# Kernel tuning notes

Hardware: AMD Instinct MI355X
Metric: run time of the kernel (lower is better)

The kernel has to match this reference:

```python
import jax, jax.numpy as jnp
import numpy as np

B, N, F_IN, H, OUT = 64, 1024, 195, 128, 64
K1, K2 = N // 2, N // 4  # ceil(0.5*N), ceil(0.5*K1)
EPS = 1e-5


def setup_inputs() -> dict:
    key = jax.random.key(0)
    ks = jax.random.split(key, 16)
    rn = lambda k, s: jax.random.normal(k, s, dtype=jnp.float32) * 0.1
    inp = {
        "input": jax.random.normal(ks[0], (B, N, F_IN), dtype=jnp.float32),
        # SAGEConv1 (195->128): lin_l (neighbors, w/ bias), lin_r (root, no bias)
        "W1l": rn(ks[1], (H, F_IN)), "b1l": jnp.zeros((H,), jnp.float32),
        "W1r": rn(ks[2], (H, F_IN)),
        # SAGPooling1 GNN = GraphConv(128->1): lin_rel (sum aggr, w/ bias), lin_root (no bias)
        "Wp1_rel": rn(ks[3], (1, H)), "bp1_rel": jnp.zeros((1,), jnp.float32),
        "Wp1_root": rn(ks[4], (1, H)),
        # SAGEConv2 (128->64)
        "W2l": rn(ks[5], (OUT, H)), "b2l": jnp.zeros((OUT,), jnp.float32),
        "W2r": rn(ks[6], (OUT, H)),
        # SAGPooling2 GNN = GraphConv(64->1)
        "Wp2_rel": rn(ks[7], (1, OUT)), "bp2_rel": jnp.zeros((1,), jnp.float32),
        "Wp2_root": rn(ks[8], (1, OUT)),
        # MLP head
        "fc1_w": rn(ks[9], (512, OUT)), "fc1_b": jnp.zeros((512,), jnp.float32),
        "bn1_g": jnp.ones((512,), jnp.float32), "bn1_b": jnp.zeros((512,), jnp.float32),
        "bn1_m": jnp.zeros((512,), jnp.float32), "bn1_v": jnp.ones((512,), jnp.float32),
        "fc2_w": rn(ks[10], (256, 512)), "fc2_b": jnp.zeros((256,), jnp.float32),
        "bn2_g": jnp.ones((256,), jnp.float32), "bn2_b": jnp.zeros((256,), jnp.float32),
        "bn2_m": jnp.zeros((256,), jnp.float32), "bn2_v": jnp.ones((256,), jnp.float32),
        "fc3_w": rn(ks[11], (2, 256)), "fc3_b": jnp.zeros((2,), jnp.float32),
    }
    return inp


def _corr_adj(x):
    # Pearson corrcoef over rows of x [B,N,F] -> boolean adjacency [B,N,N] (corr > 0.5)
    xc = x - x.mean(axis=-1, keepdims=True)
    cov = jnp.einsum("bnf,bmf->bnm", xc, xc)
    d = jnp.sqrt(jnp.clip(jnp.einsum("bnnf->bn", cov[..., None] * 0 + 0) + jnp.diagonal(cov, axis1=1, axis2=2), 1e-12))
    corr = cov / (d[:, :, None] * d[:, None, :])
    return (corr > 0.5).astype(x.dtype)  # symmetric, includes self-loops


def _sage(x, A, Wl, bl, Wr):
    # PyG SAGEConv: lin_l(mean_{j in N(i)} x_j) + lin_r(x_i)
    deg = A.sum(axis=-1, keepdims=True)
    agg = jnp.einsum("bnm,bmf->bnf", A, x) / jnp.maximum(deg, 1.0)
    return jnp.einsum("bnf,hf->bnh", agg, Wl) + bl + jnp.einsum("bnf,hf->bnh", x, Wr)


def _sagpool(x, A, Wrel, brel, Wroot, k):
    # score via GraphConv (sum aggr): lin_rel(sum_j x_j) + lin_root(x_i)
    agg = jnp.einsum("bnm,bmf->bnf", A, x)
    score = (jnp.einsum("bnf,of->bno", agg, Wrel) + brel
             + jnp.einsum("bnf,of->bno", x, Wroot))[..., 0]  # [B,N]
    top_s, idx = jax.lax.top_k(score, k)  # per-graph top-k nodes
    x_new = jnp.take_along_axis(x, idx[:, :, None], axis=1) * jnp.tanh(top_s)[:, :, None]
    A_new = jnp.take_along_axis(A, idx[:, :, None], axis=1)
    A_new = jnp.take_along_axis(A_new, idx[:, None, :], axis=2)
    return x_new, A_new


def _bn_eval(x, g, b, m, v):
    return g * (x - m) * jax.lax.rsqrt(v + EPS) + b


def reference(input, W1l, b1l, W1r, Wp1_rel, bp1_rel, Wp1_root,
              W2l, b2l, W2r, Wp2_rel, bp2_rel, Wp2_root,
              fc1_w, fc1_b, bn1_g, bn1_b, bn1_m, bn1_v,
              fc2_w, fc2_b, bn2_g, bn2_b, bn2_m, bn2_v,
              fc3_w, fc3_b):
    A = _corr_adj(input)                                   # [B,N,N]
    x = jax.nn.relu(_sage(input, A, W1l, b1l, W1r))        # [B,N,128]
    x, A = _sagpool(x, A, Wp1_rel, bp1_rel, Wp1_root, K1)  # [B,K1,128]
    x = jax.nn.relu(_sage(x, A, W2l, b2l, W2r))            # [B,K1,64]
    x, A = _sagpool(x, A, Wp2_rel, bp2_rel, Wp2_root, K2)  # [B,K2,64]
    x = x.mean(axis=1)                                     # global mean pool -> [B,64]
    x = _bn_eval(jax.nn.relu(x @ fc1_w.T + fc1_b), bn1_g, bn1_b, bn1_m, bn1_v)
    x = _bn_eval(jax.nn.relu(x @ fc2_w.T + fc2_b), bn2_g, bn2_b, bn2_m, bn2_v)
    x = x @ fc3_w.T + fc3_b
    return jax.nn.softmax(x, axis=1)
```

## Files before the change

kernel.cpp:

```cpp
#include <hip/hip_runtime.h>
#include <cstdint>


typedef __bf16 bf16x8 __attribute__((ext_vector_type(8)));
typedef float  floatx4 __attribute__((ext_vector_type(4)));

#define MFMA_BF16(a, b, c) __builtin_amdgcn_mfma_f32_16x16x32_bf16((a), (b), (c), 0, 0, 0)

static constexpr int BATCH = 64, NNODE = 1024, FIN = 195, FPAD = 224;
static constexpr int HD = 128, OD = 64, KP1 = 512, KP2 = 256;

static constexpr size_t OFF_GHI   = 0;
static constexpr size_t OFF_GLO   = 8388608;
static constexpr size_t OFF_A1B   = 16777216;
static constexpr size_t OFF_YR2   = 18874368;
static constexpr size_t OFF_X2    = 35651584;
static constexpr size_t OFF_XHI   = 0;
static constexpr size_t OFF_XLO   = 29360128;
static constexpr size_t OFF_ABITS = 58720256;
static constexpr size_t OFF_X1    = 67108864;
static constexpr size_t OFF_P1    = 100663296;
static constexpr size_t OFF_Q1    = OFF_P1 + 262144;
static constexpr size_t OFF_IDX1  = OFF_Q1 + 262144;
static constexpr size_t OFF_GATE1 = OFF_IDX1 + 131072;
static constexpr size_t OFF_P2    = OFF_GATE1 + 131072;
static constexpr size_t OFF_Q2    = OFF_P2 + 131072;
static constexpr size_t OFF_W1HI  = OFF_Q2 + 131072;
static constexpr size_t OFF_W1LO  = OFF_W1HI + 114688;
static constexpr size_t OFF_W2HI  = OFF_W1LO + 114688;
static constexpr size_t OFF_W2LO  = OFF_W2HI + 32768;
static constexpr size_t OFF_XHAT  = 102760448;
static constexpr size_t OFF_YR1   = 102760448;

__global__ __launch_bounds__(256) void prep_pack_kernel(
    const float* __restrict__ x, __bf16* __restrict__ xhi,
    __bf16* __restrict__ xlo, __bf16* __restrict__ xhat,
    const float* __restrict__ W1l, const float* __restrict__ W1r,
    __bf16* __restrict__ hi1, __bf16* __restrict__ lo1,
    const float* __restrict__ W2l, const float* __restrict__ W2r,
    __bf16* __restrict__ hi2, __bf16* __restrict__ lo2) {
  int bid = blockIdx.x;
  if (bid < 16384) {
    int row  = bid * 4 + (threadIdx.x >> 6);
    int lane = threadIdx.x & 63;
    const float* xr = x + (long)row * FIN;
    int k0 = lane * 4;
    float v[4];
#pragma unroll
    for (int i = 0; i < 4; ++i) v[i] = (k0 + i < FIN) ? xr[k0 + i] : 0.f;
    float s = v[0] + v[1] + v[2] + v[3];
#pragma unroll
    for (int o = 32; o; o >>= 1) s += __shfl_xor(s, o);
    float mean = s * (1.f / (float)FIN);
    float c[4], ss = 0.f;
#pragma unroll
    for (int i = 0; i < 4; ++i) {
      c[i] = (k0 + i < FIN) ? (v[i] - mean) : 0.f;
      ss += c[i] * c[i];
    }
#pragma unroll
    for (int o = 32; o; o >>= 1) ss += __shfl_xor(ss, o);
    float inv = rsqrtf(fmaxf(ss, 1e-12f));
    if (k0 < FPAD) {
      __bf16 hi4[4], lo4[4], hat4[4];
#pragma unroll
      for (int i = 0; i < 4; ++i) {
        float xv = (k0 + i < FIN) ? v[i] : 0.f;
        __bf16 h = (__bf16)xv;
        hi4[i] = h;
        lo4[i] = (__bf16)(xv - (float)h);
        hat4[i] = (__bf16)(c[i] * inv);
      }
      long base = (long)row * FPAD + k0;
      *(uint2*)&xhi[base]  = *(const uint2*)hi4;
      *(uint2*)&xlo[base]  = *(const uint2*)lo4;
      *(uint2*)&xhat[base] = *(const uint2*)hat4;
    }
  } else if (bid < 16384 + 224) {
    int idx = (bid - 16384) * 256 + threadIdx.x;
    int h = idx / FPAD, k = idx % FPAD;
    float v = 0.f;
    if (k < FIN) v = (h < HD) ? W1l[h * FIN + k] : W1r[(h - HD) * FIN + k];
    __bf16 a = (__bf16)v;
    hi1[idx] = a;
    lo1[idx] = (__bf16)(v - (float)a);
  } else {
    int idx = (bid - 16384 - 224) * 256 + threadIdx.x;
    int h = idx / HD, k = idx % HD;
    float v = (h < OD) ? W2l[h * HD + k] : W2r[(h - OD) * HD + k];
    __bf16 a = (__bf16)v;
    hi2[idx] = a;
    lo2[idx] = (__bf16)(v - (float)a);
  }
}

static constexpr int CK = 40;
__global__ __launch_bounds__(256) void corr_kernel(
    const __bf16* __restrict__ xhat, unsigned short* __restrict__ Abits) {
  __shared__ __align__(16) __bf16 sI[128 * CK];
  __shared__ __align__(16) __bf16 sJ[128 * CK];
  int bid = blockIdx.x;
  int xcd = bid & 7;
  int m = bid >> 3;
  int b = xcd + ((m & 7) << 3);
  int rem = m >> 3, bi = 0;
  while (rem >= 8 - bi) { rem -= 8 - bi; ++bi; }
  int bj = bi + rem;
  int i0 = bi * 128, j0 = bj * 128;
  const __bf16* Xb = xhat + (long)b * NNODE * FPAD;
  int lane = threadIdx.x & 63, wave = threadIdx.x >> 6;
  int wi = (wave >> 1) * 64, wj = (wave & 1) * 64;
  int lr = lane & 15, lk = (lane >> 4) * 8;
  int strow = threadIdx.x & 127;
  int stc = (threadIdx.x >> 7) * 8;
  floatx4 zero = {0.f, 0.f, 0.f, 0.f};
  floatx4 acc[4][4];
#pragma unroll
  for (int i = 0; i < 4; ++i)
#pragma unroll
    for (int j = 0; j < 4; ++j) acc[i][j] = zero;
  for (int kk = 0; kk < 7; ++kk) {
    int k0 = kk * 32;
    __syncthreads();
    {
      const __bf16* gI = Xb + (long)(i0 + strow) * FPAD + k0;
      const __bf16* gJ = Xb + (long)(j0 + strow) * FPAD + k0;
      *(uint4*)&sI[strow * CK + stc]      = *(const uint4*)(gI + stc);
      *(uint4*)&sI[strow * CK + stc + 16] = *(const uint4*)(gI + stc + 16);
      *(uint4*)&sJ[strow * CK + stc]      = *(const uint4*)(gJ + stc);
      *(uint4*)&sJ[strow * CK + stc + 16] = *(const uint4*)(gJ + stc + 16);
    }
    __syncthreads();
    bf16x8 af[4], bf[4];
#pragma unroll
    for (int t = 0; t < 4; ++t) {
      af[t] = *(const bf16x8*)&sI[(wi + t * 16 + lr) * CK + lk];
      bf[t] = *(const bf16x8*)&sJ[(wj + t * 16 + lr) * CK + lk];
    }
#pragma unroll
    for (int ti = 0; ti < 4; ++ti)
#pragma unroll
      for (int tj = 0; tj < 4; ++tj)
        acc[ti][tj] = MFMA_BF16(af[ti], bf[tj], acc[ti][tj]);
  }
#pragma unroll
  for (int ti = 0; ti < 4; ++ti)
#pragma unroll
    for (int tj = 0; tj < 4; ++tj) {
      floatx4 a = acc[ti][tj];
      unsigned long long m0 = __ballot(a[0] > 0.5f);
      unsigned long long m1 = __ballot(a[1] > 0.5f);
      unsigned long long m2 = __ballot(a[2] > 0.5f);
      unsigned long long m3 = __ballot(a[3] > 0.5f);
      if (lane < 16) {
        unsigned long long mm = (lane & 2) ? ((lane & 1) ? m3 : m2)
                                           : ((lane & 1) ? m1 : m0);
        unsigned short piece = (unsigned short)(mm >> ((lane >> 2) * 16));
        int grow = i0 + wi + ti * 16 + lane;
        int gcol = (j0 + wj + tj * 16) >> 4;
        Abits[((long)b * NNODE + grow) * 64 + gcol] = piece;
      }
    }
}

template <int K, int NCOL>
__global__ __launch_bounds__(512, 2) void gemm_split_kernel(
    const __bf16* __restrict__ Ahi, const __bf16* __restrict__ Alo,
    const __bf16* __restrict__ Bhi, const __bf16* __restrict__ Blo,
    float* __restrict__ C, int mblocks,
    unsigned long long* __restrict__ A64, int ntrans) {
  constexpr int ldc = NCOL * 128;
  int bid = blockIdx.x;
  if (bid >= mblocks * NCOL) {
    int t = bid - mblocks * NCOL;
    if (t >= ntrans || threadIdx.x >= 256) return;
    int b = t / 28, pi = t % 28;
    int rem = pi, rb = 1;
    while (rem >= rb) { rem -= rb; ++rb; }
    int cb = rem;
    int wave = threadIdx.x >> 6, lane = threadIdx.x & 63;
    int dr = rb * 2 + (wave >> 1);
    int dc = cb * 2 + (wave & 1);
    long base = (long)b * NNODE;
    unsigned long long xv = A64[(base + dc * 64 + lane) * 16 + dr];
    const unsigned long long M1  = 0x5555555555555555ULL;
    const unsigned long long M2  = 0x3333333333333333ULL;
    const unsigned long long M4  = 0x0F0F0F0F0F0F0F0FULL;
    const unsigned long long M8  = 0x00FF00FF00FF00FFULL;
    const unsigned long long M16 = 0x0000FFFF0000FFFFULL;
    const unsigned long long M32 = 0x00000000FFFFFFFFULL;
#define TSTEP(Kk, M)                                                      \
    {                                                                     \
      unsigned long long y = __shfl_xor(xv, Kk);                          \
      xv = ((lane & Kk) == 0) ? ((xv & (M)) | ((y & (M)) << Kk))          \
                              : ((xv & ~(M)) | ((y & ~(M)) >> Kk));       \
    }
    TSTEP(1, M1) TSTEP(2, M2) TSTEP(4, M4) TSTEP(8, M8) TSTEP(16, M16) TSTEP(32, M32)
#undef TSTEP
    A64[(base + dr * 64 + lane) * 16 + dc] = xv;
    return;
  }
  int mrow, col;
  if (NCOL == 2) {
    int xcd = bid & 7;
    int q = bid >> 3;
    col = q & 1;
    mrow = (xcd << 6) + (q >> 1);
  } else {
    mrow = bid;
    col = 0;
  }
  long row0 = (long)mrow * 128;
  int col0 = col * 128;
  int lane = threadIdx.x & 63, wave = threadIdx.x >> 6;
  int wi = (wave >> 1) * 32, wj = (wave & 1) * 64;
  int lr = lane & 15, lk = (lane >> 4) * 8;
  const __bf16* pAh = Ahi + (row0 + wi + lr) * (long)K + lk;
  const __bf16* pAl = Alo + (row0 + wi + lr) * (long)K + lk;
  const __bf16* pBh = Bhi + (long)(col0 + wj + lr) * K + lk;
  const __bf16* pBl = Blo + (long)(col0 + wj + lr) * K + lk;
  floatx4 zero = {0.f, 0.f, 0.f, 0.f};
  floatx4 acc[2][4];
#pragma unroll
  for (int i = 0; i < 2; ++i)
#pragma unroll
    for (int j = 0; j < 4; ++j) acc[i][j] = zero;
#pragma unroll
  for (int kk = 0; kk < (K >> 5); ++kk) {
    int k0 = kk * 32;
    bf16x8 ah[2], al[2], bh[4], bl[4];
#pragma unroll
    for (int t = 0; t < 2; ++t) {
      ah[t] = *(const bf16x8*)(pAh + (long)t * 16 * K + k0);
      al[t] = *(const bf16x8*)(pAl + (long)t * 16 * K + k0);
    }
#pragma unroll
    for (int t = 0; t < 4; ++t) {
      bh[t] = *(const bf16x8*)(pBh + (long)t * 16 * K + k0);
      bl[t] = *(const bf16x8*)(pBl + (long)t * 16 * K + k0);
    }
#pragma unroll
    for (int tj = 0; tj < 4; ++tj)
#pragma unroll
      for (int ti = 0; ti < 2; ++ti) {
        acc[ti][tj] = MFMA_BF16(ah[ti], bh[tj], acc[ti][tj]);
        acc[ti][tj] = MFMA_BF16(ah[ti], bl[tj], acc[ti][tj]);
        acc[ti][tj] = MFMA_BF16(al[ti], bh[tj], acc[ti][tj]);
      }
  }
#pragma unroll
  for (int ti = 0; ti < 2; ++ti)
#pragma unroll
    for (int tj = 0; tj < 4; ++tj)
#pragma unroll
      for (int rr = 0; rr < 4; ++rr) {
        long grow = row0 + wi + ti * 16 + (lane >> 4) * 4 + rr;
        int gcol = col0 + wj + tj * 16 + (lane & 15);
        C[grow * ldc + gcol] = acc[ti][tj][rr];
      }
}

__global__ __launch_bounds__(256) void sage1_kernel(
    const unsigned int* __restrict__ Abits32, const float* __restrict__ YR1,
    const float* __restrict__ b1l, const float* __restrict__ Wrel,
    const float* __restrict__ Wroot, float* __restrict__ x1,
    float* __restrict__ p1, float* __restrict__ q1) {
  int half = threadIdx.x >> 7;
  int node = blockIdx.x * 2 + half;
  int b = node >> 10;
  int h = threadIdx.x & 127;
  __shared__ int list[2][1024];
  __shared__ int s_deg[2];
  __shared__ float redp[2][2], redq[2][2];
  if (h < 32) {
    unsigned int word = Abits32[(long)node * 32 + h];
    int cnt = __popc(word);
    int off = cnt;
#pragma unroll
    for (int o = 1; o < 32; o <<= 1) {
      int v = __shfl_up(off, o);
      if (h >= o) off += v;
    }
    off -= cnt;
    if (h == 31) s_deg[half] = off + cnt;
    int basei = h * 32;
    while (word) {
      int t = __ffs(word) - 1;
      word &= word - 1;
      list[half][off++] = basei + t;
    }
  }
  __syncthreads();
  int deg = s_deg[half];
  long ybase = (long)(b << 10) * 256;
  float accv = 0.f;
  for (int d = 0; d < deg; ++d)
    accv += YR1[ybase + (long)list[half][d] * 256 + h];
  float R = YR1[(long)node * 256 + 128 + h];
  float v = accv / (float)(deg < 1 ? 1 : deg) + b1l[h] + R;
  v = fmaxf(v, 0.f);
  x1[(long)node * 128 + h] = v;
  float pv = v * Wrel[h], qv = v * Wroot[h];
#pragma unroll
  for (int o = 32; o; o >>= 1) { pv += __shfl_xor(pv, o); qv += __shfl_xor(qv, o); }
  int wv = h >> 6, lane = h & 63;
  if (lane == 0) { redp[half][wv] = pv; redq[half][wv] = qv; }
  __syncthreads();
  if (h == 0) {
    p1[node] = redp[half][0] + redp[half][1];
    q1[node] = redq[half][0] + redq[half][1];
  }
}

__global__ void scoretopk_kernel(const unsigned int* __restrict__ bits32,
                                 const float* __restrict__ p,
                                 const float* __restrict__ q,
                                 const float* __restrict__ brel,
                                 int* __restrict__ idx_out,
                                 float* __restrict__ gate_out,
                                 int nwords, int rpb_shift, int k) {
  int b = blockIdx.x, tid = threadIdx.x;
  int row = (b << rpb_shift) + tid;
  const unsigned int* wptr = bits32 + (long)row * nwords;
  const float* pb = p + ((long)b << rpb_shift);
  float s = q[row] + brel[0];
  for (int w = 0; w < nwords; ++w) {
    unsigned int word = wptr[w];
    while (word) {
      int t = __ffs(word) - 1;
      word &= word - 1;
      s += pb[w * 32 + t];
    }
  }
  unsigned int fb = __float_as_uint(s);
  unsigned int key = (fb & 0x80000000u) ? ~fb : (fb | 0x80000000u);
  __shared__ int hist[256];
  __shared__ unsigned int sh_prefix;
  __shared__ int sh_target, cnt_gt, cnt_eq, outpos;
  if (tid == 0) { sh_prefix = 0; sh_target = k; cnt_gt = 0; cnt_eq = 0; outpos = 0; }
  for (int shift = 24; shift >= 0; shift -= 8) {
    if (tid < 256) hist[tid] = 0;
    __syncthreads();
    unsigned int prefix = sh_prefix;
    bool inset = (shift == 24) || ((key >> (shift + 8)) == (prefix >> (shift + 8)));
    if (inset) atomicAdd(&hist[(key >> shift) & 255], 1);
    __syncthreads();
    if (tid < 64) {
      int lane = tid;
      int bb0 = hist[255 - 4 * lane];
      int bb1 = hist[254 - 4 * lane];
      int bb2 = hist[253 - 4 * lane];
      int bb3 = hist[252 - 4 * lane];
      int c0 = bb0, c1 = c0 + bb1, c2 = c1 + bb2, c3 = c2 + bb3;
      int incl = c3;
#pragma unroll
      for (int o = 1; o < 64; o <<= 1) {
        int v = __shfl_up(incl, o);
        if (lane >= o) incl += v;
      }
      int excl = incl - c3;
      int target = sh_target;
      int cum[4] = {excl + c0, excl + c1, excl + c2, excl + c3};
      int prev = excl;
#pragma unroll
      for (int i = 0; i < 4; ++i) {
        if (cum[i] >= target && prev < target) {
          int bin = 255 - (4 * lane + i);
          sh_prefix = prefix | ((unsigned int)bin << shift);
          sh_target = target - prev;
        }
        prev = cum[i];
      }
    }
    __syncthreads();
  }
  unsigned int T = sh_prefix;
  if (key > T) atomicAdd(&cnt_gt, 1);
  __syncthreads();
  int E = k - cnt_gt;
  bool sel = (key > T);
  if (!sel && key == T) sel = (atomicAdd(&cnt_eq, 1) < E);
  if (sel) {
    int posn = atomicAdd(&outpos, 1);
    idx_out[b * k + posn] = tid;
    gate_out[b * k + posn] = tanhf(s);
  }
}

__global__ __launch_bounds__(256) void gather_kernel(
    const float* __restrict__ x1, const int* __restrict__ idx,
    const float* __restrict__ gate, __bf16* __restrict__ ghi,
    __bf16* __restrict__ glo, const unsigned int* __restrict__ Abits32,
    unsigned long long* __restrict__ A1bits) {
  int bid = blockIdx.x;
  if (bid < 16384) {
    long e = (long)bid * 256 + threadIdx.x;
    int h = (int)(e & 127);
    int i = (int)((e >> 7) & 511);
    int b = (int)(e >> 16);
    int srow = idx[(b << 9) + i];
    float v = x1[((long)(b << 10) + srow) * 128 + h] * gate[(b << 9) + i];
    __bf16 a = (__bf16)v;
    ghi[e] = a;
    glo[e] = (__bf16)(v - (float)a);
  } else {
    int gi = (bid - 16384) * 4 + (threadIdx.x >> 6);
    int lane = threadIdx.x & 63;
    int b = gi >> 9;
    int srow = idx[gi];
    const unsigned int* src = Abits32 + ((long)(b << 10) + srow) * 32;
    const int* idxb = idx + (b << 9);
#pragma unroll
    for (int t = 0; t < 8; ++t) {
      int cj = idxb[t * 64 + lane];
      int bit = (src[cj >> 5] >> (cj & 31)) & 1;
      unsigned long long m = __ballot(bit);
      if (lane == 0) A1bits[(long)gi * 8 + t] = m;
    }
  }
}

__global__ __launch_bounds__(256) void sage2_kernel(
    const unsigned int* __restrict__ A1b32, const float* __restrict__ YR2,
    const float* __restrict__ b2l, const float* __restrict__ Wrel,
    const float* __restrict__ Wroot, float* __restrict__ x2,
    float* __restrict__ p2, float* __restrict__ q2) {
  int qw = threadIdx.x >> 6;
  int row = blockIdx.x * 4 + qw;
  int b = row >> 9;
  int h = threadIdx.x & 63;
  __shared__ int list[4][512];
  __shared__ int s_deg[4];
  if (h < 16) {
    unsigned int word = A1b32[(long)row * 16 + h];
    int cnt = __popc(word);
    int off = cnt;
#pragma unroll
    for (int o = 1; o < 16; o <<= 1) {
      int v = __shfl_up(off, o);
      if (h >= o) off += v;
    }
    off -= cnt;
    if (h == 15) s_deg[qw] = off + cnt;
    int basei = h * 32;
    while (word) {
      int t = __ffs(word) - 1;
      word &= word - 1;
      list[qw][off++] = basei + t;
    }
  }
  __syncthreads();
  int deg = s_deg[qw];
  long ybase = (long)(b << 9) * 128;
  float accv = 0.f;
  for (int d = 0; d < deg; ++d)
    accv += YR2[ybase + (long)list[qw][d] * 128 + h];
  float R = YR2[(long)row * 128 + 64 + h];
  float v = fmaxf(accv / (float)(deg < 1 ? 1 : deg) + b2l[h] + R, 0.f);
  x2[(long)row * 64 + h] = v;
  float pv = v * Wrel[h], qv = v * Wroot[h];
#pragma unroll
  for (int o = 32; o; o >>= 1) { pv += __shfl_xor(pv, o); qv += __shfl_xor(qv, o); }
  if (h == 0) { p2[row] = pv; q2[row] = qv; }
}

__global__ __launch_bounds__(512) void scoretopk_head_kernel(
    const unsigned int* __restrict__ A1b32, const float* __restrict__ p2,
    const float* __restrict__ q2, const float* __restrict__ brel,
    const float* __restrict__ x2, const float* __restrict__ fc1_w,
    const float* __restrict__ fc1_b, const float* __restrict__ g1,
    const float* __restrict__ bb1, const float* __restrict__ m1,
    const float* __restrict__ v1, const float* __restrict__ fc2_w,
    const float* __restrict__ fc2_b, const float* __restrict__ g2,
    const float* __restrict__ bb2, const float* __restrict__ m2,
    const float* __restrict__ v2, const float* __restrict__ fc3_w,
    const float* __restrict__ fc3_b, float* __restrict__ out) {
  int b = blockIdx.x, tid = threadIdx.x;
  int row = (b << 9) + tid;
  const unsigned int* wptr = A1b32 + (long)row * 16;
  const float* pb = p2 + ((long)b << 9);
  float s = q2[row] + brel[0];
  for (int w = 0; w < 16; ++w) {
    unsigned int word = wptr[w];
    while (word) {
      int t = __ffs(word) - 1;
      word &= word - 1;
      s += pb[w * 32 + t];
    }
  }
  constexpr int k = KP2;
  unsigned int fb = __float_as_uint(s);
  unsigned int key = (fb & 0x80000000u) ? ~fb : (fb | 0x80000000u);
  __shared__ int hist[256];
  __shared__ int idx2s[256];
  __shared__ float gate2s[256];
  __shared__ unsigned int sh_prefix;
  __shared__ int sh_target, cnt_gt, cnt_eq, outpos;
  if (tid == 0) { sh_prefix = 0; sh_target = k; cnt_gt = 0; cnt_eq = 0; outpos = 0; }
  for (int shift = 24; shift >= 0; shift -= 8) {
    if (tid < 256) hist[tid] = 0;
    __syncthreads();
    unsigned int prefix = sh_prefix;
    bool inset = (shift == 24) || ((key >> (shift + 8)) == (prefix >> (shift + 8)));
    if (inset) atomicAdd(&hist[(key >> shift) & 255], 1);
    __syncthreads();
    if (tid < 64) {
      int lane = tid;
      int bb0 = hist[255 - 4 * lane];
      int bb1 = hist[254 - 4 * lane];
      int bb2 = hist[253 - 4 * lane];
      int bb3 = hist[252 - 4 * lane];
      int c0 = bb0, c1 = c0 + bb1, c2 = c1 + bb2, c3 = c2 + bb3;
      int incl = c3;
#pragma unroll
      for (int o = 1; o < 64; o <<= 1) {
        int v = __shfl_up(incl, o);
        if (lane >= o) incl += v;
      }
      int excl = incl - c3;
      int target = sh_target;
      int cum[4] = {excl + c0, excl + c1, excl + c2, excl + c3};
      int prev = excl;
#pragma unroll
      for (int i = 0; i < 4; ++i) {
        if (cum[i] >= target && prev < target) {
          int bin = 255 - (4 * lane + i);
          sh_prefix = prefix | ((unsigned int)bin << shift);
          sh_target = target - prev;
        }
        prev = cum[i];
      }
    }
    __syncthreads();
  }
  unsigned int T = sh_prefix;
  if (key > T) atomicAdd(&cnt_gt, 1);
  __syncthreads();
  int E = k - cnt_gt;
  bool sel = (key > T);
  if (!sel && key == T) sel = (atomicAdd(&cnt_eq, 1) < E);
  if (sel) {
    int posn = atomicAdd(&outpos, 1);
    idx2s[posn] = tid;
    gate2s[posn] = tanhf(s);
  }
  __syncthreads();
  __shared__ float part[8][64];
  __shared__ float pooled[64];
  __shared__ float h1[512];
  __shared__ float h2[256];
  __shared__ float zz[2];
  int h = tid & 63, grp = tid >> 6;
  float sp = 0.f;
  for (int i = grp * 32; i < grp * 32 + 32; ++i) {
    int si = idx2s[i];
    sp += x2[((long)(b << 9) + si) * 64 + h] * gate2s[i];
  }
  part[grp][h] = sp;
  __syncthreads();
  if (tid < 64) {
    float t = 0.f;
#pragma unroll
    for (int g = 0; g < 8; ++g) t += part[g][tid];
    pooled[tid] = t * (1.f / 256.f);
  }
  __syncthreads();
  {
    float z = fc1_b[tid];
    for (int j = 0; j < 64; ++j) z += pooled[j] * fc1_w[tid * 64 + j];
    z = fmaxf(z, 0.f);
    h1[tid] = g1[tid] * (z - m1[tid]) * rsqrtf(v1[tid] + 1e-5f) + bb1[tid];
  }
  __syncthreads();
  if (tid < 256) {
    float z = fc2_b[tid];
    for (int j = 0; j < 512; ++j) z += h1[j] * fc2_w[tid * 512 + j];
    z = fmaxf(z, 0.f);
    h2[tid] = g2[tid] * (z - m2[tid]) * rsqrtf(v2[tid] + 1e-5f) + bb2[tid];
  }
  __syncthreads();
  if (tid < 2) {
    float z = fc3_b[tid];
    for (int j = 0; j < 256; ++j) z += h2[j] * fc3_w[tid * 256 + j];
    zz[tid] = z;
  }
  __syncthreads();
  if (tid == 0) {
    float mx = fmaxf(zz[0], zz[1]);
    float e0 = expf(zz[0] - mx), e1 = expf(zz[1] - mx);
    float inv = 1.f / (e0 + e1);
    out[b * 2 + 0] = e0 * inv;
    out[b * 2 + 1] = e1 * inv;
  }
}

extern "C" void kernel_launch(void* const* d_in, const int* in_sizes, int n_in,
                              void* d_out, int out_size, void* d_ws, size_t ws_size,
                              hipStream_t stream) {
  (void)in_sizes; (void)n_in; (void)out_size; (void)ws_size;
  const float* input   = (const float*)d_in[0];
  const float* W1l     = (const float*)d_in[1];
  const float* b1l     = (const float*)d_in[2];
  const float* W1r     = (const float*)d_in[3];
  const float* Wp1_rel = (const float*)d_in[4];
  const float* bp1_rel = (const float*)d_in[5];
  const float* Wp1_root= (const float*)d_in[6];
  const float* W2l     = (const float*)d_in[7];
  const float* b2l     = (const float*)d_in[8];
  const float* W2r     = (const float*)d_in[9];
  const float* Wp2_rel = (const float*)d_in[10];
  const float* bp2_rel = (const float*)d_in[11];
  const float* Wp2_root= (const float*)d_in[12];
  const float* fc1_w   = (const float*)d_in[13];
  const float* fc1_b   = (const float*)d_in[14];
  const float* bn1_g   = (const float*)d_in[15];
  const float* bn1_b   = (const float*)d_in[16];
  const float* bn1_m   = (const float*)d_in[17];
  const float* bn1_v   = (const float*)d_in[18];
  const float* fc2_w   = (const float*)d_in[19];
  const float* fc2_b   = (const float*)d_in[20];
  const float* bn2_g   = (const float*)d_in[21];
  const float* bn2_b   = (const float*)d_in[22];
  const float* bn2_m   = (const float*)d_in[23];
  const float* bn2_v   = (const float*)d_in[24];
  const float* fc3_w   = (const float*)d_in[25];
  const float* fc3_b   = (const float*)d_in[26];

  char* ws = (char*)d_ws;
  __bf16* xhi   = (__bf16*)(ws + OFF_XHI);
  __bf16* xlo   = (__bf16*)(ws + OFF_XLO);
  __bf16* xhat  = (__bf16*)(ws + OFF_XHAT);
  unsigned short* Abits = (unsigned short*)(ws + OFF_ABITS);
  const unsigned int* Abits32 = (const unsigned int*)(ws + OFF_ABITS);
  unsigned long long* A64 = (unsigned long long*)(ws + OFF_ABITS);
  float* YR1    = (float*)(ws + OFF_YR1);
  float* x1     = (float*)(ws + OFF_X1);
  float* p1     = (float*)(ws + OFF_P1);
  float* q1     = (float*)(ws + OFF_Q1);
  int*   idx1   = (int*)(ws + OFF_IDX1);
  float* gate1  = (float*)(ws + OFF_GATE1);
  float* p2     = (float*)(ws + OFF_P2);
  float* q2     = (float*)(ws + OFF_Q2);
  __bf16* w1hi  = (__bf16*)(ws + OFF_W1HI);
  __bf16* w1lo  = (__bf16*)(ws + OFF_W1LO);
  __bf16* w2hi  = (__bf16*)(ws + OFF_W2HI);
  __bf16* w2lo  = (__bf16*)(ws + OFF_W2LO);
  __bf16* ghi   = (__bf16*)(ws + OFF_GHI);
  __bf16* glo   = (__bf16*)(ws + OFF_GLO);
  unsigned long long* A1bits = (unsigned long long*)(ws + OFF_A1B);
  const unsigned int* A1b32  = (const unsigned int*)(ws + OFF_A1B);
  float* YR2    = (float*)(ws + OFF_YR2);
  float* x2     = (float*)(ws + OFF_X2);
  float* out    = (float*)d_out;

  prep_pack_kernel<<<16672, 256, 0, stream>>>(input, xhi, xlo, xhat,
                                              W1l, W1r, w1hi, w1lo,
                                              W2l, W2r, w2hi, w2lo);
  corr_kernel<<<2304, 256, 0, stream>>>(xhat, Abits);
  gemm_split_kernel<224, 2><<<1024 + 1792, 512, 0, stream>>>(
      xhi, xlo, w1hi, w1lo, YR1, 512, A64, 1792);
  sage1_kernel<<<32768, 256, 0, stream>>>(Abits32, YR1, b1l, Wp1_rel, Wp1_root, x1, p1, q1);
  scoretopk_kernel<<<64, 1024, 0, stream>>>(Abits32, p1, q1, bp1_rel, idx1, gate1,
                                            32, 10, KP1);
  gather_kernel<<<24576, 256, 0, stream>>>(x1, idx1, gate1, ghi, glo, Abits32, A1bits);
  gemm_split_kernel<128, 1><<<256, 512, 0, stream>>>(
      ghi, glo, w2hi, w2lo, YR2, 256, nullptr, 0);
  sage2_kernel<<<8192, 256, 0, stream>>>(A1b32, YR2, b2l, Wp2_rel, Wp2_root, x2, p2, q2);
  scoretopk_head_kernel<<<64, 512, 0, stream>>>(A1b32, p2, q2, bp2_rel, x2,
                                                fc1_w, fc1_b, bn1_g, bn1_b, bn1_m, bn1_v,
                                                fc2_w, fc2_b, bn2_g, bn2_b, bn2_m, bn2_v,
                                                fc3_w, fc3_b, out);
}
```

Baseline: 389.9 us.

## Compute correlation adjacency with FP8 MFMA and enlarge split-GEMM wave tiles

Normalized rows for the correlation matrix are now stored as FP8 e4m3 instead of bf16, and corr_kernel uses the fp8 16x16x32 MFMA. This halves the staging bytes and LDS traffic for the adjacency build. The threshold at 0.5 may flip for correlations near the boundary, because FP8 keeps only a 3-bit mantissa, so the result can diverge from the reference. Separately, gemm_split runs with 256 threads per block, each wave computing a 64x64 tile instead of 32x64, which raises register use and data reuse per wave. The YR1 offset is moved so it no longer aliases the xhat buffer.

```diff
diff --git a/kernel.cpp b/kernel.cpp
--- a/kernel.cpp
+++ b/kernel.cpp
@@ -1,4 +1,5 @@
 #include <hip/hip_runtime.h>
+#include <hip/hip_fp8.h>
 #include <cstdint>
 
 
@@ -6,6 +7,7 @@
 typedef float  floatx4 __attribute__((ext_vector_type(4)));
 
 #define MFMA_BF16(a, b, c) __builtin_amdgcn_mfma_f32_16x16x32_bf16((a), (b), (c), 0, 0, 0)
+#define MFMA_FP8(a, b, c)  __builtin_amdgcn_mfma_f32_16x16x32_fp8_fp8((a), (b), (c), 0, 0, 0)
 
 static constexpr int BATCH = 64, NNODE = 1024, FIN = 195, FPAD = 224;
 static constexpr int HD = 128, OD = 64, KP1 = 512, KP2 = 256;
@@ -30,11 +32,16 @@
 static constexpr size_t OFF_W2HI  = OFF_W1LO + 114688;
 static constexpr size_t OFF_W2LO  = OFF_W2HI + 32768;
 static constexpr size_t OFF_XHAT  = 102760448;
-static constexpr size_t OFF_YR1   = 102760448;
+static constexpr size_t OFF_YR1   = 102760448 + 16777216;
+
+static __device__ __forceinline__ unsigned char to_fp8(float v) {
+  __hip_fp8_e4m3 q(v);
+  return *(unsigned char*)&q;
+}
 
 __global__ __launch_bounds__(256) void prep_pack_kernel(
     const float* __restrict__ x, __bf16* __restrict__ xhi,
-    __bf16* __restrict__ xlo, __bf16* __restrict__ xhat,
+    __bf16* __restrict__ xlo, unsigned char* __restrict__ xhat8,
     const float* __restrict__ W1l, const float* __restrict__ W1r,
     __bf16* __restrict__ hi1, __bf16* __restrict__ lo1,
     const float* __restrict__ W2l, const float* __restrict__ W2r,
@@ -62,19 +69,20 @@
     for (int o = 32; o; o >>= 1) ss += __shfl_xor(ss, o);
     float inv = rsqrtf(fmaxf(ss, 1e-12f));
     if (k0 < FPAD) {
-      __bf16 hi4[4], lo4[4], hat4[4];
+      __bf16 hi4[4], lo4[4];
+      unsigned char h8[4];
 #pragma unroll
       for (int i = 0; i < 4; ++i) {
         float xv = (k0 + i < FIN) ? v[i] : 0.f;
         __bf16 h = (__bf16)xv;
         hi4[i] = h;
         lo4[i] = (__bf16)(xv - (float)h);
-        hat4[i] = (__bf16)(c[i] * inv);
+        h8[i] = to_fp8(c[i] * inv);
       }
       long base = (long)row * FPAD + k0;
-      *(uint2*)&xhi[base]  = *(const uint2*)hi4;
-      *(uint2*)&xlo[base]  = *(const uint2*)lo4;
-      *(uint2*)&xhat[base] = *(const uint2*)hat4;
+      *(uint2*)&xhi[base] = *(const uint2*)hi4;
+      *(uint2*)&xlo[base] = *(const uint2*)lo4;
+      *(unsigned int*)&xhat8[base] = *(const unsigned int*)h8;
     }
   } else if (bid < 16384 + 224) {
     int idx = (bid - 16384) * 256 + threadIdx.x;
@@ -94,11 +102,11 @@
   }
 }
 
-static constexpr int CK = 40;
+static constexpr int CKB = 48;
 __global__ __launch_bounds__(256) void corr_kernel(
-    const __bf16* __restrict__ xhat, unsigned short* __restrict__ Abits) {
-  __shared__ __align__(16) __bf16 sI[128 * CK];
-  __shared__ __align__(16) __bf16 sJ[128 * CK];
+    const unsigned char* __restrict__ xhat8, unsigned short* __restrict__ Abits) {
+  __shared__ __align__(16) unsigned char sI[128 * CKB];
+  __shared__ __align__(16) unsigned char sJ[128 * CKB];
   int bid = blockIdx.x;
   int xcd = bid & 7;
   int m = bid >> 3;
@@ -107,12 +115,12 @@
   while (rem >= 8 - bi) { rem -= 8 - bi; ++bi; }
   int bj = bi + rem;
   int i0 = bi * 128, j0 = bj * 128;
-  const __bf16* Xb = xhat + (long)b * NNODE * FPAD;
+  const unsigned char* Xb = xhat8 + (long)b * NNODE * FPAD;
   int lane = threadIdx.x & 63, wave = threadIdx.x >> 6;
   int wi = (wave >> 1) * 64, wj = (wave & 1) * 64;
-  int lr = lane & 15, lk = (lane >> 4) * 8;
+  int lr = lane & 15, lk8 = (lane >> 4) * 8;
   int strow = threadIdx.x & 127;
-  int stc = (threadIdx.x >> 7) * 8;
+  int sbuf = threadIdx.x >> 7;
   floatx4 zero = {0.f, 0.f, 0.f, 0.f};
   floatx4 acc[4][4];
 #pragma unroll
@@ -123,25 +131,23 @@
     int k0 = kk * 32;
     __syncthreads();
     {
-      const __bf16* gI = Xb + (long)(i0 + strow) * FPAD + k0;
-      const __bf16* gJ = Xb + (long)(j0 + strow) * FPAD + k0;
-      *(uint4*)&sI[strow * CK + stc]      = *(const uint4*)(gI + stc);
-      *(uint4*)&sI[strow * CK + stc + 16] = *(const uint4*)(gI + stc + 16);
-      *(uint4*)&sJ[strow * CK + stc]      = *(const uint4*)(gJ + stc);
-      *(uint4*)&sJ[strow * CK + stc + 16] = *(const uint4*)(gJ + stc + 16);
-    }
-    __syncthreads();
-    bf16x8 af[4], bf[4];
+      unsigned char* dst = (sbuf ? sJ : sI) + strow * CKB;
+      const unsigned char* src = Xb + (long)((sbuf ? j0 : i0) + strow) * FPAD + k0;
+      *(uint4*)(dst)      = *(const uint4*)(src);
+      *(uint4*)(dst + 16) = *(const uint4*)(src + 16);
+    }
+    __syncthreads();
+    long long af[4], bf[4];
 #pragma unroll
     for (int t = 0; t < 4; ++t) {
-      af[t] = *(const bf16x8*)&sI[(wi + t * 16 + lr) * CK + lk];
-      bf[t] = *(const bf16x8*)&sJ[(wj + t * 16 + lr) * CK + lk];
+      af[t] = *(const long long*)&sI[(wi + t * 16 + lr) * CKB + lk8];
+      bf[t] = *(const long long*)&sJ[(wj + t * 16 + lr) * CKB + lk8];
     }
 #pragma unroll
     for (int ti = 0; ti < 4; ++ti)
 #pragma unroll
       for (int tj = 0; tj < 4; ++tj)
-        acc[ti][tj] = MFMA_BF16(af[ti], bf[tj], acc[ti][tj]);
+        acc[ti][tj] = MFMA_FP8(af[ti], bf[tj], acc[ti][tj]);
   }
 #pragma unroll
   for (int ti = 0; ti < 4; ++ti)
@@ -164,7 +170,7 @@
 }
 
 template <int K, int NCOL>
-__global__ __launch_bounds__(512, 2) void gemm_split_kernel(
+__global__ __launch_bounds__(256, 2) void gemm_split_kernel(
     const __bf16* __restrict__ Ahi, const __bf16* __restrict__ Alo,
     const __bf16* __restrict__ Bhi, const __bf16* __restrict__ Blo,
     float* __restrict__ C, int mblocks,
@@ -173,7 +179,7 @@
   int bid = blockIdx.x;
   if (bid >= mblocks * NCOL) {
     int t = bid - mblocks * NCOL;
-    if (t >= ntrans || threadIdx.x >= 256) return;
+    if (t >= ntrans) return;
     int b = t / 28, pi = t % 28;
     int rem = pi, rb = 1;
     while (rem >= rb) { rem -= rb; ++rb; }
@@ -213,43 +219,40 @@
   long row0 = (long)mrow * 128;
   int col0 = col * 128;
   int lane = threadIdx.x & 63, wave = threadIdx.x >> 6;
-  int wi = (wave >> 1) * 32, wj = (wave & 1) * 64;
+  int wi = (wave >> 1) * 64, wj = (wave & 1) * 64;
   int lr = lane & 15, lk = (lane >> 4) * 8;
   const __bf16* pAh = Ahi + (row0 + wi + lr) * (long)K + lk;
   const __bf16* pAl = Alo + (row0 + wi + lr) * (long)K + lk;
   const __bf16* pBh = Bhi + (long)(col0 + wj + lr) * K + lk;
   const __bf16* pBl = Blo + (long)(col0 + wj + lr) * K + lk;
   floatx4 zero = {0.f, 0.f, 0.f, 0.f};
-  floatx4 acc[2][4];
-#pragma unroll
-  for (int i = 0; i < 2; ++i)
+  floatx4 acc[4][4];
+#pragma unroll
+  for (int i = 0; i < 4; ++i)
 #pragma unroll
     for (int j = 0; j < 4; ++j) acc[i][j] = zero;
 #pragma unroll
   for (int kk = 0; kk < (K >> 5); ++kk) {
     int k0 = kk * 32;
-    bf16x8 ah[2], al[2], bh[4], bl[4];
-#pragma unroll
-    for (int t = 0; t < 2; ++t) {
+    bf16x8 ah[4], al[4], bh[4], bl[4];
+#pragma unroll
+    for (int t = 0; t < 4; ++t) {
       ah[t] = *(const bf16x8*)(pAh + (long)t * 16 * K + k0);
       al[t] = *(const bf16x8*)(pAl + (long)t * 16 * K + k0);
-    }
-#pragma unroll
-    for (int t = 0; t < 4; ++t) {
       bh[t] = *(const bf16x8*)(pBh + (long)t * 16 * K + k0);
       bl[t] = *(const bf16x8*)(pBl + (long)t * 16 * K + k0);
     }
 #pragma unroll
     for (int tj = 0; tj < 4; ++tj)
 #pragma unroll
-      for (int ti = 0; ti < 2; ++ti) {
+      for (int ti = 0; ti < 4; ++ti) {
         acc[ti][tj] = MFMA_BF16(ah[ti], bh[tj], acc[ti][tj]);
         acc[ti][tj] = MFMA_BF16(ah[ti], bl[tj], acc[ti][tj]);
         acc[ti][tj] = MFMA_BF16(al[ti], bh[tj], acc[ti][tj]);
       }
   }
 #pragma unroll
-  for (int ti = 0; ti < 2; ++ti)
+  for (int ti = 0; ti < 4; ++ti)
 #pragma unroll
     for (int tj = 0; tj < 4; ++tj)
 #pragma unroll
@@ -629,7 +632,7 @@
   char* ws = (char*)d_ws;
   __bf16* xhi   = (__bf16*)(ws + OFF_XHI);
   __bf16* xlo   = (__bf16*)(ws + OFF_XLO);
-  __bf16* xhat  = (__bf16*)(ws + OFF_XHAT);
+  unsigned char* xhat8 = (unsigned char*)(ws + OFF_XHAT);
   unsigned short* Abits = (unsigned short*)(ws + OFF_ABITS);
   const unsigned int* Abits32 = (const unsigned int*)(ws + OFF_ABITS);
   unsigned long long* A64 = (unsigned long long*)(ws + OFF_ABITS);
@@ -653,17 +656,17 @@
   float* x2     = (float*)(ws + OFF_X2);
   float* out    = (float*)d_out;
 
-  prep_pack_kernel<<<16672, 256, 0, stream>>>(input, xhi, xlo, xhat,
+  prep_pack_kernel<<<16672, 256, 0, stream>>>(input, xhi, xlo, xhat8,
                                               W1l, W1r, w1hi, w1lo,
                                               W2l, W2r, w2hi, w2lo);
-  corr_kernel<<<2304, 256, 0, stream>>>(xhat, Abits);
-  gemm_split_kernel<224, 2><<<1024 + 1792, 512, 0, stream>>>(
+  corr_kernel<<<2304, 256, 0, stream>>>(xhat8, Abits);
+  gemm_split_kernel<224, 2><<<1024 + 1792, 256, 0, stream>>>(
       xhi, xlo, w1hi, w1lo, YR1, 512, A64, 1792);
   sage1_kernel<<<32768, 256, 0, stream>>>(Abits32, YR1, b1l, Wp1_rel, Wp1_root, x1, p1, q1);
   scoretopk_kernel<<<64, 1024, 0, stream>>>(Abits32, p1, q1, bp1_rel, idx1, gate1,
                                             32, 10, KP1);
   gather_kernel<<<24576, 256, 0, stream>>>(x1, idx1, gate1, ghi, glo, Abits32, A1bits);
-  gemm_split_kernel<128, 1><<<256, 512, 0, stream>>>(
+  gemm_split_kernel<128, 1><<<256, 256, 0, stream>>>(
       ghi, glo, w2hi, w2lo, YR2, 256, nullptr, 0);
   sage2_kernel<<<8192, 256, 0, stream>>>(A1b32, YR2, b2l, Wp2_rel, Wp2_root, x2, p2, q2);
   scoretopk_head_kernel<<<64, 512, 0, stream>>>(A1b32, p2, q2, bp2_rel, x2,
```

Measured after the change: 366.3 us. 6.0% less time.
